# Kernel tuning notes

Hardware: AMD Instinct MI355X
Metric: run time of the kernel (lower is better)

Reference implementation:

```python
import jax, jax.numpy as jnp
import numpy as np

SCALE = 0.2
ASPECT = 1.0
ORIGIN = (0.5, 0.5)
AREA_THRESH = 400


def setup_inputs() -> dict:
    key = jax.random.key(0)
    kb, ki, kp, kd = jax.random.split(key, 4)
    B, N, H, W = 16, 16, 640, 640
    k1, k2, k3, k4 = jax.random.split(kb, 4)
    ymin = jax.random.uniform(k1, (B, N)) * 280.0
    xmin = jax.random.uniform(k2, (B, N)) * 280.0
    h = 150.0 + jax.random.uniform(k3, (B, N)) * 170.0
    w = 150.0 + jax.random.uniform(k4, (B, N)) * 170.0
    boxes = jnp.stack([ymin, xmin, h, w], axis=-1)  # [B,N,4] = [ymin,xmin,h,w]
    images = jax.random.uniform(ki, (B, H, W, 3), dtype=jnp.float32)
    patch = jax.random.uniform(kp, (300, 300, 3), dtype=jnp.float32)
    transform_decisions = jax.random.bernoulli(kd, 0.5, (B, N, 3))  # rot90, flip_lr, flip_ud
    return {"boxes": boxes, "images": images, "patch": patch,
            "transform_decisions": transform_decisions}


def _bilinear_sample(patch, sy, sx):
    # tf.image.resize (v2 bilinear, half-pixel centers) expressed as a gather.
    Hp, Wp, _ = patch.shape
    sy = jnp.clip(sy, 0.0, Hp - 1.0)
    sx = jnp.clip(sx, 0.0, Wp - 1.0)
    y0 = jnp.floor(sy).astype(jnp.int32)
    x0 = jnp.floor(sx).astype(jnp.int32)
    y1 = jnp.minimum(y0 + 1, Hp - 1)
    x1 = jnp.minimum(x0 + 1, Wp - 1)
    wy = (sy - y0)[..., None]
    wx = (sx - x0)[..., None]
    p00 = patch[y0, x0]; p01 = patch[y0, x1]
    p10 = patch[y1, x0]; p11 = patch[y1, x1]
    top = p00 * (1.0 - wx) + p01 * wx
    bot = p10 * (1.0 - wx) + p11 * wx
    return top * (1.0 - wy) + bot * wy  # [H,W,C]


def _patch_boxes(boxes, H, W):
    # Patcher.create(): place a scale*h square patch at box origin, clamp to image.
    ymin, xmin, h, w = (boxes[..., i] for i in range(4))
    ph = h * SCALE
    pw = ASPECT * ph
    y0 = ymin + h * ORIGIN[1]
    x0 = xmin + w * ORIGIN[0]
    y0 = jnp.where(y0 + ph > H, H - ph, y0)
    x0 = jnp.where(x0 + pw > W, W - pw, x0)
    return jnp.stack([y0, x0, ph, pw], axis=-1)


def _forward(boxes, images, patch, transform_decisions):
    B, H, W, C = images.shape
    Hp, Wp, _ = patch.shape
    pboxes = _patch_boxes(boxes, float(H), float(W))  # [B,N,4] float
    bi = pboxes.astype(jnp.int32)                     # tf.cast truncation
    valid = (bi[..., 2] * bi[..., 3]) > AREA_THRESH   # area filter (mask, not ragged)
    Y = jnp.arange(H)[:, None]
    X = jnp.arange(W)[None, :]

    def apply_patch(img, carry):
        box, dec, v = carry
        y0i, x0i = box[0], box[1]
        s = jnp.maximum(box[2], 1)  # square side (aspect=1); guard div-by-zero
        iy = Y - y0i                 # local patch coords of every image pixel
        ix = X - x0i
        inside = (iy >= 0) & (iy < s) & (ix >= 0) & (ix < s) & v
        iyc = jnp.clip(iy, 0, s - 1)
        ixc = jnp.clip(ix, 0, s - 1)
        d0, d1, d2 = dec[0], dec[1], dec[2]
        iy2 = jnp.where(d2, s - 1 - iyc, iyc)  # invert flip_up_down
        ix2 = jnp.where(d1, s - 1 - ixc, ixc)  # invert flip_left_right
        ry = jnp.where(d0, ix2, iy2)           # invert rot90 (CCW): out[i,j]=in[j,s-1-i]
        rx = jnp.where(d0, s - 1 - iy2, ix2)
        sf = s.astype(jnp.float32)
        sy = (ry.astype(jnp.float32) + 0.5) * (Hp / sf) - 0.5  # half-pixel resize map
        sx = (rx.astype(jnp.float32) + 0.5) * (Wp / sf) - 0.5
        sample = _bilinear_sample(patch, sy, sx)
        img = jnp.where(inside[..., None], sample, img)  # overwrite region
        return img, None

    def per_image(img, box_b, dec_b, valid_b):
        img, _ = jax.lax.scan(apply_patch, img, (box_b, dec_b, valid_b))
        return img

    images_out = jax.vmap(per_image)(images, bi, transform_decisions, valid)
    return images_out, pboxes


def reference(boxes, images, patch, transform_decisions):
    return _forward(boxes, images, patch, transform_decisions)
```

## Files before the change

kernel.cpp:

```cpp
#include <hip/hip_runtime.h>
#include <hip/hip_bf16.h>

#define B_  16
#define N_  16
#define H_  640
#define W_  640
#define HP_ 300
#define WP_ 300
#define IMG_FLOATS (H_ * W_ * 3)
#define ALL_FLOATS (B_ * IMG_FLOATS)
#define PBOX_OFF   ALL_FLOATS
#define IMG_F4     (IMG_FLOATS / 4)
#define F4_PER_BLOCK 768
#define BLOCKS_PER_IMG (IMG_F4 / F4_PER_BLOCK)
#define CELLS_PER_IMG (H_ * W_ / 64)
#define CM_OFF_BYTES (B_ * N_ * 4 * 4)


__global__ __launch_bounds__(256) void prep_kernel(
    const float* __restrict__ boxes,
    const unsigned char* __restrict__ dec_raw,
    float* __restrict__ pboxes_out,
    int* __restrict__ info,
    unsigned short* __restrict__ cm,
    int build_cm)
{
    int b = blockIdx.x;
    int t = threadIdx.x;
    __shared__ int s_nz, s_fp;
    __shared__ int ly0[N_], lx0[N_], ls[N_], lfl[N_];
    if (t == 0) { s_nz = 0; s_fp = 0; }
    __syncthreads();
    int nz = 0, fp = 0;
    for (int i = t; i < B_ * N_ * 3; i += 256) {
        unsigned char by = dec_raw[i];
        if ((i & 3) && by) nz = 1;
        if (by == 0x3F || by == 0x80) fp = 1;
    }
    if (nz) atomicOr(&s_nz, 1);
    if (fp) atomicOr(&s_fp, 1);
    __syncthreads();
    int mode = !s_nz ? 1 : (s_fp ? 2 : 0);

    if (t < N_) {
        int e = b * N_ + t;
        float ymin = boxes[e*4+0], xmin = boxes[e*4+1];
        float h = boxes[e*4+2], w = boxes[e*4+3];
        float ph = h * 0.2f;
        float pw = 1.0f * ph;
        float y0 = ymin + h * 0.5f;
        float x0 = xmin + w * 0.5f;
        if (y0 + ph > (float)H_) y0 = (float)H_ - ph;
        if (x0 + pw > (float)W_) x0 = (float)W_ - pw;
        pboxes_out[e*4+0] = y0; pboxes_out[e*4+1] = x0;
        pboxes_out[e*4+2] = ph; pboxes_out[e*4+3] = pw;

        int y0i = (int)y0, x0i = (int)x0;
        int phi = (int)ph, pwi = (int)pw;
        int valid = (phi * pwi) > 400;
        int s = phi > 1 ? phi : 1;

        int d0, d1, d2;
        if (mode == 0) {
            d0 = dec_raw[e*3+0] != 0; d1 = dec_raw[e*3+1] != 0; d2 = dec_raw[e*3+2] != 0;
        } else if (mode == 1) {
            const int* di = (const int*)dec_raw;
            d0 = di[e*3+0] != 0; d1 = di[e*3+1] != 0; d2 = di[e*3+2] != 0;
        } else {
            const float* df = (const float*)dec_raw;
            d0 = df[e*3+0] != 0.0f; d1 = df[e*3+1] != 0.0f; d2 = df[e*3+2] != 0.0f;
        }
        int flags = valid | (d0 << 1) | (d1 << 2) | (d2 << 3);
        ly0[t] = y0i; lx0[t] = x0i; ls[t] = s; lfl[t] = flags;
        int* ei = info + e * 4;
        ei[0] = y0i; ei[1] = x0i; ei[2] = s; ei[3] = flags;
    }
    __syncthreads();

    if (build_cm) {
        unsigned short* cmb = cm + b * CELLS_PER_IMG;
        for (int c = t; c < CELLS_PER_IMG; c += 256) {
            int gy  = c / (W_ / 64);
            int gx0 = (c - gy * (W_ / 64)) * 64;
            unsigned m16 = 0;
            for (int m = 0; m < N_; ++m) {
                if ((lfl[m] & 1) &&
                    (unsigned)(gy - ly0[m]) < (unsigned)ls[m] &&
                    lx0[m] < gx0 + 64 && lx0[m] + ls[m] > gx0)
                    m16 |= 1u << m;
            }
            cmb[c] = (unsigned short)m16;
        }
    }
}

__device__ __forceinline__ int sample_px(
    int p, unsigned mask,
    const int* ly0, const int* lx0, const int* ls, const int* lfl,
    const float* __restrict__ patch,
    float& cr, float& cg, float& cb)
{
    int gy = p / W_;
    int gx = p - gy * W_;
    while (mask) {
        int m = 31 - __clz(mask);
        int s = ls[m];
        int ry = gy - ly0[m], rx = gx - lx0[m];
        if ((unsigned)ry < (unsigned)s && (unsigned)rx < (unsigned)s) {
            int fl = lfl[m];
            int iy2 = (fl & 8) ? (s - 1 - ry) : ry;
            int ix2 = (fl & 4) ? (s - 1 - rx) : rx;
            int ty  = (fl & 2) ? ix2 : iy2;
            int tx  = (fl & 2) ? (s - 1 - iy2) : ix2;
            float sf  = (float)s;
            float sc  = (float)HP_ / sf;
            float sy = ((float)ty + 0.5f) * sc - 0.5f;
            float sx = ((float)tx + 0.5f) * sc - 0.5f;
            sy = fminf(fmaxf(sy, 0.0f), (float)(HP_ - 1));
            sx = fminf(fmaxf(sx, 0.0f), (float)(WP_ - 1));
            int yy0 = (int)sy;
            int xx0 = (int)sx;
            int yy1 = yy0 + 1 < HP_ - 1 ? yy0 + 1 : HP_ - 1;
            int xx1 = xx0 + 1 < WP_ - 1 ? xx0 + 1 : WP_ - 1;
            float wy = sy - (float)yy0;
            float wx = sx - (float)xx0;
            const float* p00 = patch + (yy0 * WP_ + xx0) * 3;
            const float* p01 = patch + (yy0 * WP_ + xx1) * 3;
            const float* p10 = patch + (yy1 * WP_ + xx0) * 3;
            const float* p11 = patch + (yy1 * WP_ + xx1) * 3;
            float t0 = p00[0]*(1.f-wx) + p01[0]*wx;
            float b0 = p10[0]*(1.f-wx) + p11[0]*wx;
            cr = t0*(1.f-wy) + b0*wy;
            float t1 = p00[1]*(1.f-wx) + p01[1]*wx;
            float b1 = p10[1]*(1.f-wx) + p11[1]*wx;
            cg = t1*(1.f-wy) + b1*wy;
            float t2 = p00[2]*(1.f-wx) + p01[2]*wx;
            float b2 = p10[2]*(1.f-wx) + p11[2]*wx;
            cb = t2*(1.f-wy) + b2*wy;
            return 1;
        }
        mask &= ~(1u << m);
    }
    return 0;
}

__device__ __forceinline__ float4 process_f4(
    float4 v, int f,
    const unsigned short* __restrict__ cmb,
    const int* ly0, const int* lx0, const int* ls, const int* lfl,
    const float* __restrict__ patch, int use_tab)
{
    int wlo = f & ~63;
    int whi = wlo + 63;
    int px_lo = wlo + wlo / 3;
    int px_hi = (4 * whi + 3) / 3;
    unsigned mask;
    if (use_tab) {
        int c0 = px_lo >> 6, c1 = px_hi >> 6;
        mask = (unsigned)cmb[c0] | (unsigned)cmb[c1];
        if (c1 == c0 + 2) mask |= (unsigned)cmb[c0 + 1];
    } else {
        int ry0 = px_lo / W_, ry1 = px_hi / W_;
        int cx0, cx1;
        if (ry0 == ry1) { cx0 = px_lo - ry0 * W_; cx1 = px_hi - ry0 * W_; }
        else            { cx0 = 0; cx1 = W_ - 1; }
        mask = 0;
        for (int m = 0; m < N_; ++m)
            if ((lfl[m] & 1) && ly0[m] <= ry1 && ly0[m] + ls[m] > ry0 &&
                lx0[m] <= cx1 && lx0[m] + ls[m] > cx0)
                mask |= 1u << m;
    }
    if (!mask) return v;

    int p0 = f + f / 3;
    float c00, c01, c02, c10, c11, c12;
    int h0 = sample_px(p0,     mask, ly0, lx0, ls, lfl, patch, c00, c01, c02);
    int h1 = sample_px(p0 + 1, mask, ly0, lx0, ls, lfl, patch, c10, c11, c12);
    if (!(h0 | h1)) return v;

    int r = f % 3;
    float vv0 = v.x, vv1 = v.y, vv2 = v.z, vv3 = v.w;
    if (r == 0) {
        if (h0) { vv0 = c00; vv1 = c01; vv2 = c02; }
        if (h1) { vv3 = c10; }
    } else if (r == 1) {
        if (h0) { vv0 = c01; vv1 = c02; }
        if (h1) { vv2 = c10; vv3 = c11; }
    } else {
        if (h0) { vv0 = c02; }
        if (h1) { vv1 = c10; vv2 = c11; vv3 = c12; }
    }
    return make_float4(vv0, vv1, vv2, vv3);
}

__global__ __launch_bounds__(256) void fused_kernel(
    const float4* __restrict__ images4,
    const float*  __restrict__ patch,
    const int*    __restrict__ info,
    const unsigned short* __restrict__ cm,
    float4*       __restrict__ out4,
    int use_tab)
{
    int blk = blockIdx.x;
    int b = blk / BLOCKS_PER_IMG;
    int blkLocal = blk - b * BLOCKS_PER_IMG;
    int t = threadIdx.x;

    __shared__ int ly0[N_], lx0[N_], ls[N_], lfl[N_];
    if (t < N_) {
        const int* ei = info + (b * N_ + t) * 4;
        ly0[t] = ei[0]; lx0[t] = ei[1]; ls[t] = ei[2]; lfl[t] = ei[3];
    }
    __syncthreads();

    const float4* ib = images4 + (size_t)b * IMG_F4;
    float4*       ob = out4    + (size_t)b * IMG_F4;
    const unsigned short* cmb = cm + b * CELLS_PER_IMG;

    int f0 = blkLocal * F4_PER_BLOCK + t;
    float4 v0 = ib[f0];
    float4 v1 = ib[f0 + 256];
    float4 v2 = ib[f0 + 512];

    v0 = process_f4(v0, f0,       cmb, ly0, lx0, ls, lfl, patch, use_tab);
    v1 = process_f4(v1, f0 + 256, cmb, ly0, lx0, ls, lfl, patch, use_tab);
    v2 = process_f4(v2, f0 + 512, cmb, ly0, lx0, ls, lfl, patch, use_tab);

    ob[f0]       = v0;
    ob[f0 + 256] = v1;
    ob[f0 + 512] = v2;
}

extern "C" void kernel_launch(void* const* d_in, const int* in_sizes, int n_in,
                              void* d_out, int out_size, void* d_ws, size_t ws_size,
                              hipStream_t stream) {
    const float*         boxes   = (const float*)d_in[0];
    const float*         images  = (const float*)d_in[1];
    const float*         patch   = (const float*)d_in[2];
    const unsigned char* dec_raw = (const unsigned char*)d_in[3];

    float* out    = (float*)d_out;
    float* pboxes = out + PBOX_OFF;
    int*   info   = (int*)d_ws;
    unsigned short* cm = (unsigned short*)((char*)d_ws + CM_OFF_BYTES);
    size_t need = CM_OFF_BYTES + (size_t)B_ * CELLS_PER_IMG * sizeof(unsigned short);
    int use_tab = (ws_size >= need) ? 1 : 0;

    prep_kernel<<<B_, 256, 0, stream>>>(boxes, dec_raw, pboxes, info, cm, use_tab);
    fused_kernel<<<B_ * BLOCKS_PER_IMG, 256, 0, stream>>>(
        (const float4*)images, patch, info, cm, (float4*)out, use_tab);
}
```

Measured before the change: 164.5 us.

## Per-wave chunk masks, 8 float4 per thread, nontemporal stores

Rebuilds the coverage table per 64-float4 chunk (one wavefront's contiguous span) so each thread looks up one precomputed mask per float4 instead of combining 2-3 pixel-cell masks. Raises work per block to 2048 float4 with all 8 loads issued up front for more memory-level parallelism. Drops the shared-memory staging and barrier of the box info in favour of direct int4 reads, and writes output with nontemporal stores. The copy is bandwidth bound, so the aim is better streaming efficiency, at the cost of fewer blocks and more registers per thread.

```diff
diff --git a/kernel.cpp b/kernel.cpp
--- a/kernel.cpp
+++ b/kernel.cpp
@@ -11,10 +11,12 @@
 #define ALL_FLOATS (B_ * IMG_FLOATS)
 #define PBOX_OFF   ALL_FLOATS
 #define IMG_F4     (IMG_FLOATS / 4)
-#define F4_PER_BLOCK 768
+#define F4_PER_BLOCK 2048
 #define BLOCKS_PER_IMG (IMG_F4 / F4_PER_BLOCK)
-#define CELLS_PER_IMG (H_ * W_ / 64)
-#define CM_OFF_BYTES (B_ * N_ * 4 * 4)
+#define CHUNKS_PER_IMG (IMG_F4 / 64)
+#define CM_OFF_BYTES 4096
+
+typedef float f4v __attribute__((ext_vector_type(4)));
 
 
 __global__ __launch_bounds__(256) void prep_kernel(
@@ -78,16 +80,26 @@
     __syncthreads();
 
     if (build_cm) {
-        unsigned short* cmb = cm + b * CELLS_PER_IMG;
-        for (int c = t; c < CELLS_PER_IMG; c += 256) {
-            int gy  = c / (W_ / 64);
-            int gx0 = (c - gy * (W_ / 64)) * 64;
+        unsigned short* cmb = cm + b * CHUNKS_PER_IMG;
+        for (int c = t; c < CHUNKS_PER_IMG; c += 256) {
+            int px_lo = (256 * c) / 3;
+            int px_hi = (256 * c + 255) / 3;
+            int ry0 = px_lo / W_, ry1 = px_hi / W_;
+            int cx0 = px_lo - ry0 * W_;
+            int cx1 = px_hi - ry1 * W_;
             unsigned m16 = 0;
             for (int m = 0; m < N_; ++m) {
-                if ((lfl[m] & 1) &&
-                    (unsigned)(gy - ly0[m]) < (unsigned)ls[m] &&
-                    lx0[m] < gx0 + 64 && lx0[m] + ls[m] > gx0)
-                    m16 |= 1u << m;
+                if (!(lfl[m] & 1)) continue;
+                int s = ls[m];
+                int hit = 0;
+                int hi0 = (ry0 == ry1) ? cx1 : (W_ - 1);
+                if ((unsigned)(ry0 - ly0[m]) < (unsigned)s &&
+                    lx0[m] <= hi0 && lx0[m] + s > cx0) hit = 1;
+                if (ry1 != ry0) {
+                    if ((unsigned)(ry1 - ly0[m]) < (unsigned)s &&
+                        lx0[m] <= cx1 && lx0[m] + s > 0) hit = 1;
+                }
+                if (hit) m16 |= 1u << m;
             }
             cmb[c] = (unsigned short)m16;
         }
@@ -95,8 +107,7 @@
 }
 
 __device__ __forceinline__ int sample_px(
-    int p, unsigned mask,
-    const int* ly0, const int* lx0, const int* ls, const int* lfl,
+    int p, unsigned mask, const int4* __restrict__ binfo,
     const float* __restrict__ patch,
     float& cr, float& cg, float& cb)
 {
@@ -104,10 +115,11 @@
     int gx = p - gy * W_;
     while (mask) {
         int m = 31 - __clz(mask);
-        int s = ls[m];
-        int ry = gy - ly0[m], rx = gx - lx0[m];
+        int4 e = binfo[m];
+        int s = e.z;
+        int ry = gy - e.x, rx = gx - e.y;
         if ((unsigned)ry < (unsigned)s && (unsigned)rx < (unsigned)s) {
-            int fl = lfl[m];
+            int fl = e.w;
             int iy2 = (fl & 8) ? (s - 1 - ry) : ry;
             int ix2 = (fl & 4) ? (s - 1 - rx) : rx;
             int ty  = (fl & 2) ? ix2 : iy2;
@@ -144,61 +156,59 @@
     return 0;
 }
 
-__device__ __forceinline__ float4 process_f4(
-    float4 v, int f,
-    const unsigned short* __restrict__ cmb,
-    const int* ly0, const int* lx0, const int* ls, const int* lfl,
-    const float* __restrict__ patch, int use_tab)
-{
-    int wlo = f & ~63;
-    int whi = wlo + 63;
-    int px_lo = wlo + wlo / 3;
-    int px_hi = (4 * whi + 3) / 3;
-    unsigned mask;
-    if (use_tab) {
-        int c0 = px_lo >> 6, c1 = px_hi >> 6;
-        mask = (unsigned)cmb[c0] | (unsigned)cmb[c1];
-        if (c1 == c0 + 2) mask |= (unsigned)cmb[c0 + 1];
-    } else {
-        int ry0 = px_lo / W_, ry1 = px_hi / W_;
-        int cx0, cx1;
-        if (ry0 == ry1) { cx0 = px_lo - ry0 * W_; cx1 = px_hi - ry0 * W_; }
-        else            { cx0 = 0; cx1 = W_ - 1; }
-        mask = 0;
-        for (int m = 0; m < N_; ++m)
-            if ((lfl[m] & 1) && ly0[m] <= ry1 && ly0[m] + ls[m] > ry0 &&
-                lx0[m] <= cx1 && lx0[m] + ls[m] > cx0)
-                mask |= 1u << m;
-    }
-    if (!mask) return v;
-
+__device__ __forceinline__ f4v proc_f4(
+    f4v v, int f, unsigned mask,
+    const int4* __restrict__ binfo,
+    const float* __restrict__ patch)
+{
     int p0 = f + f / 3;
     float c00, c01, c02, c10, c11, c12;
-    int h0 = sample_px(p0,     mask, ly0, lx0, ls, lfl, patch, c00, c01, c02);
-    int h1 = sample_px(p0 + 1, mask, ly0, lx0, ls, lfl, patch, c10, c11, c12);
+    int h0 = sample_px(p0,     mask, binfo, patch, c00, c01, c02);
+    int h1 = sample_px(p0 + 1, mask, binfo, patch, c10, c11, c12);
     if (!(h0 | h1)) return v;
 
     int r = f % 3;
-    float vv0 = v.x, vv1 = v.y, vv2 = v.z, vv3 = v.w;
     if (r == 0) {
-        if (h0) { vv0 = c00; vv1 = c01; vv2 = c02; }
-        if (h1) { vv3 = c10; }
+        if (h0) { v.x = c00; v.y = c01; v.z = c02; }
+        if (h1) { v.w = c10; }
     } else if (r == 1) {
-        if (h0) { vv0 = c01; vv1 = c02; }
-        if (h1) { vv2 = c10; vv3 = c11; }
+        if (h0) { v.x = c01; v.y = c02; }
+        if (h1) { v.z = c10; v.w = c11; }
     } else {
-        if (h0) { vv0 = c02; }
-        if (h1) { vv1 = c10; vv2 = c11; vv3 = c12; }
-    }
-    return make_float4(vv0, vv1, vv2, vv3);
+        if (h0) { v.x = c02; }
+        if (h1) { v.y = c10; v.z = c11; v.w = c12; }
+    }
+    return v;
+}
+
+__device__ __forceinline__ unsigned chunk_mask_inline(
+    int c, const int4* __restrict__ binfo)
+{
+    int px_lo = (256 * c) / 3;
+    int px_hi = (256 * c + 255) / 3;
+    int ry0 = px_lo / W_, ry1 = px_hi / W_;
+    int cx0 = px_lo - ry0 * W_;
+    int cx1 = px_hi - ry1 * W_;
+    unsigned m16 = 0;
+    for (int m = 0; m < N_; ++m) {
+        int4 e = binfo[m];
+        if (!(e.w & 1)) continue;
+        int s = e.z;
+        int hit = 0;
+        int hi0 = (ry0 == ry1) ? cx1 : (W_ - 1);
+        if ((unsigned)(ry0 - e.x) < (unsigned)s && e.y <= hi0 && e.y + s > cx0) hit = 1;
+        if (ry1 != ry0 && (unsigned)(ry1 - e.x) < (unsigned)s && e.y <= cx1 && e.y + s > 0) hit = 1;
+        if (hit) m16 |= 1u << m;
+    }
+    return m16;
 }
 
 __global__ __launch_bounds__(256) void fused_kernel(
-    const float4* __restrict__ images4,
-    const float*  __restrict__ patch,
-    const int*    __restrict__ info,
+    const f4v* __restrict__ images4,
+    const float* __restrict__ patch,
+    const int4* __restrict__ info,
     const unsigned short* __restrict__ cm,
-    float4*       __restrict__ out4,
+    f4v* __restrict__ out4,
     int use_tab)
 {
     int blk = blockIdx.x;
@@ -206,29 +216,33 @@
     int blkLocal = blk - b * BLOCKS_PER_IMG;
     int t = threadIdx.x;
 
-    __shared__ int ly0[N_], lx0[N_], ls[N_], lfl[N_];
-    if (t < N_) {
-        const int* ei = info + (b * N_ + t) * 4;
-        ly0[t] = ei[0]; lx0[t] = ei[1]; ls[t] = ei[2]; lfl[t] = ei[3];
-    }
-    __syncthreads();
-
-    const float4* ib = images4 + (size_t)b * IMG_F4;
-    float4*       ob = out4    + (size_t)b * IMG_F4;
-    const unsigned short* cmb = cm + b * CELLS_PER_IMG;
-
-    int f0 = blkLocal * F4_PER_BLOCK + t;
-    float4 v0 = ib[f0];
-    float4 v1 = ib[f0 + 256];
-    float4 v2 = ib[f0 + 512];
-
-    v0 = process_f4(v0, f0,       cmb, ly0, lx0, ls, lfl, patch, use_tab);
-    v1 = process_f4(v1, f0 + 256, cmb, ly0, lx0, ls, lfl, patch, use_tab);
-    v2 = process_f4(v2, f0 + 512, cmb, ly0, lx0, ls, lfl, patch, use_tab);
-
-    ob[f0]       = v0;
-    ob[f0 + 256] = v1;
-    ob[f0 + 512] = v2;
+    const int4* binfo = info + b * N_;
+    const unsigned short* cmb = cm + b * CHUNKS_PER_IMG;
+
+    size_t ibase = (size_t)b * IMG_F4 + (size_t)blkLocal * F4_PER_BLOCK + t;
+    int    fbase = blkLocal * F4_PER_BLOCK + t;
+    int    cbase = blkLocal * 32 + (t >> 6);
+
+    unsigned mk[8];
+    if (use_tab) {
+        #pragma unroll
+        for (int j = 0; j < 8; ++j) mk[j] = cmb[cbase + 4 * j];
+    } else {
+        #pragma unroll
+        for (int j = 0; j < 8; ++j) mk[j] = chunk_mask_inline(cbase + 4 * j, binfo);
+    }
+
+    f4v v[8];
+    #pragma unroll
+    for (int j = 0; j < 8; ++j) v[j] = images4[ibase + (size_t)(j * 256)];
+
+    #pragma unroll
+    for (int j = 0; j < 8; ++j)
+        if (mk[j]) v[j] = proc_f4(v[j], fbase + j * 256, mk[j], binfo, patch);
+
+    #pragma unroll
+    for (int j = 0; j < 8; ++j)
+        __builtin_nontemporal_store(v[j], (f4v*)&out4[ibase + (size_t)(j * 256)]);
 }
 
 extern "C" void kernel_launch(void* const* d_in, const int* in_sizes, int n_in,
@@ -243,10 +257,10 @@
     float* pboxes = out + PBOX_OFF;
     int*   info   = (int*)d_ws;
     unsigned short* cm = (unsigned short*)((char*)d_ws + CM_OFF_BYTES);
-    size_t need = CM_OFF_BYTES + (size_t)B_ * CELLS_PER_IMG * sizeof(unsigned short);
+    size_t need = CM_OFF_BYTES + (size_t)B_ * CHUNKS_PER_IMG * sizeof(unsigned short);
     int use_tab = (ws_size >= need) ? 1 : 0;
 
     prep_kernel<<<B_, 256, 0, stream>>>(boxes, dec_raw, pboxes, info, cm, use_tab);
     fused_kernel<<<B_ * BLOCKS_PER_IMG, 256, 0, stream>>>(
-        (const float4*)images, patch, info, cm, (float4*)out, use_tab);
-}
+        (const f4v*)images, patch, (const int4*)info, cm, (f4v*)out, use_tab);
+}
```

Result: slower. 187.6 us (+14.0%).
